# Optimization experiments

Measured on AMD Instinct MI355X. Metric: run time of the kernel, lower is better.

The kernel has to match this reference:

```python
import jax, jax.numpy as jnp
import numpy as np

T, N, D = 64, 40, 4
H, R, K = 256, 64, 2
E = N * (N - 1)


def _xavier(key, shape):
    std = (2.0 / (shape[0] + shape[1])) ** 0.5
    return (std * jax.random.normal(key, shape)).astype(jnp.float32)


def setup_inputs() -> dict:
    ks = iter(jax.random.split(jax.random.key(0), 40))
    send, recv = np.where(np.ones((N, N)) - np.eye(N))  # fully-connected directed graph, E = N*(N-1)
    p = {}
    p['inputs'] = jax.random.normal(next(ks), (1, T, N, D), dtype=jnp.float32)
    p['node_masks'] = jnp.ones((1, T, N), dtype=jnp.float32)
    p['send_edges'] = jnp.asarray(send, dtype=jnp.int32)
    p['recv_edges'] = jnp.asarray(recv, dtype=jnp.int32)
    for name, nin in (('mlp1', D), ('mlp2', 2 * H), ('mlp3', H), ('mlp4', 3 * H)):
        p[name + '_W1'] = _xavier(next(ks), (H, nin))
        p[name + '_b1'] = jnp.full((H,), 0.1, jnp.float32)
        p[name + '_W2'] = _xavier(next(ks), (H, H))
        p[name + '_b2'] = jnp.full((H,), 0.1, jnp.float32)
    s = float(1.0 / np.sqrt(R))
    for nm in ('fwd', 'rev'):
        p[nm + '_Wih'] = jax.random.uniform(next(ks), (4 * R, H), jnp.float32, -s, s)
        p[nm + '_Whh'] = jax.random.uniform(next(ks), (4 * R, R), jnp.float32, -s, s)
        p[nm + '_bih'] = jnp.zeros((4 * R,), jnp.float32)
        p[nm + '_bhh'] = jnp.zeros((4 * R,), jnp.float32)
    p['enc_W'] = _xavier(next(ks), (K, 2 * R))
    p['enc_b'] = jnp.full((K,), 0.1, jnp.float32)
    p['prior_W'] = _xavier(next(ks), (K, R))
    p['prior_b'] = jnp.full((K,), 0.1, jnp.float32)
    return p


def _mlp(x, W1, b1, W2, b2):
    # RefNRIMLP in eval mode with no_bn=True: elu(fc2(elu(fc1(x))))
    return jax.nn.elu(jax.nn.elu(x @ W1.T + b1) @ W2.T + b2)


def _lstm(xs, Wih, Whh, bih, bhh):
    # xs: [T, E, H] -> hidden states [T, E, R]; PyTorch LSTM gate order i, f, g, o
    def step(carry, xt):
        h, c = carry
        g = xt @ Wih.T + bih + h @ Whh.T + bhh
        i, f, gg, o = jnp.split(g, 4, axis=-1)
        c = jax.nn.sigmoid(f) * c + jax.nn.sigmoid(i) * jnp.tanh(gg)
        h = jax.nn.sigmoid(o) * jnp.tanh(c)
        return (h, c), h
    Rh = Whh.shape[1]
    init = (jnp.zeros((xs.shape[1], Rh), xs.dtype), jnp.zeros((xs.shape[1], Rh), xs.dtype))
    _, hs = jax.lax.scan(step, init, xs)
    return hs


def _encode(inputs, send, recv,
            m1W1, m1b1, m1W2, m1b2, m2W1, m2b1, m2W2, m2b2,
            m3W1, m3b1, m3W2, m3b2, m4W1, m4b1, m4W2, m4b2,
            fWih, fWhh, fbih, fbhh, rWih, rWhh, rbih, rbhh,
            encW, encb, priW, prib):
    x = inputs[0]                                                  # [T, N, D]
    h = _mlp(x, m1W1, m1b1, m1W2, m1b2)                            # [T, N, H]
    e = jnp.concatenate([h[:, send], h[:, recv]], axis=-1)         # node2edge gather [T, E, 2H]
    e = _mlp(e, m2W1, m2b1, m2W2, m2b2)                            # [T, E, H]
    skip = e
    n = jnp.zeros((x.shape[0], x.shape[1], e.shape[-1]), e.dtype)
    n = n.at[:, recv].add(e)                                       # edge2node scatter-add (index_add_)
    n = _mlp(n, m3W1, m3b1, m3W2, m3b2)                            # [T, N, H]
    e = jnp.concatenate([n[:, send], n[:, recv], skip], axis=-1)   # [T, E, 3H]
    e = _mlp(e, m4W1, m4b1, m4W2, m4b2)                            # per-edge features over time [T, E, H]
    fwd_h = _lstm(e, fWih, fWhh, fbih, fbhh)                       # [T, E, R]
    rev_h = _lstm(e[::-1], rWih, rWhh, rbih, rbhh)[::-1]           # [T, E, R]
    prior = fwd_h @ priW.T + prib                                  # [T, E, K]
    enc = jnp.concatenate([fwd_h, rev_h], axis=-1) @ encW.T + encb # [T, E, K]
    return jnp.concatenate([prior, enc], axis=-1)                  # [T, E, 2K]


def reference(inputs, node_masks, send_edges, recv_edges,
              mlp1_W1, mlp1_b1, mlp1_W2, mlp1_b2,
              mlp2_W1, mlp2_b1, mlp2_W2, mlp2_b2,
              mlp3_W1, mlp3_b1, mlp3_W2, mlp3_b2,
              mlp4_W1, mlp4_b1, mlp4_W2, mlp4_b2,
              fwd_Wih, fwd_Whh, fwd_bih, fwd_bhh,
              rev_Wih, rev_Whh, rev_bih, rev_bhh,
              enc_W, enc_b, prior_W, prior_b):
    del node_masks  # all nodes present -> static fully-connected graph each step
    return _encode(inputs, send_edges, recv_edges,
                   mlp1_W1, mlp1_b1, mlp1_W2, mlp1_b2,
                   mlp2_W1, mlp2_b1, mlp2_W2, mlp2_b2,
                   mlp3_W1, mlp3_b1, mlp3_W2, mlp3_b2,
                   mlp4_W1, mlp4_b1, mlp4_W2, mlp4_b2,
                   fwd_Wih, fwd_Whh, fwd_bih, fwd_bhh,
                   rev_Wih, rev_Whh, rev_bih, rev_bhh,
                   enc_W, enc_b, prior_W, prior_b)
```

## Files before the change

kernel.cpp:

```cpp
#include <hip/hip_runtime.h>
#include <math.h>

#define T_ 64
#define N_ 40
#define D_ 4
#define H_ 256
#define R_ 64
#define E_ 1560
#define TE_ (T_*E_)
#define TN_ (T_*N_)

typedef unsigned short us;
typedef short short8 __attribute__((ext_vector_type(8)));
typedef float f32x4 __attribute__((ext_vector_type(4)));

__device__ __forceinline__ float elu_f(float x){ return x > 0.f ? x : (__expf(x) - 1.f); }
__device__ __forceinline__ float sig_f(float x){ return 1.f/(1.f+__expf(-x)); }
__device__ __forceinline__ float tanh_f(float x){ return 2.f/(1.f+__expf(-2.f*x)) - 1.f; }
__device__ __forceinline__ float dot4(float4 a, float4 b){ return a.x*b.x + a.y*b.y + a.z*b.z + a.w*b.w; }

__device__ __forceinline__ float bf2f(us u){ return __uint_as_float(((unsigned int)u) << 16); }
__device__ __forceinline__ us f2bf(float f){
    unsigned int u = __float_as_uint(f);
    u += 0x7FFFu + ((u >> 16) & 1u);
    return (us)(u >> 16);
}
__device__ __forceinline__ float4 ld4f(const float* p){ return *(const float4*)p; }
__device__ __forceinline__ float4 ld4f(const us* p){
    ushort4 v = *(const ushort4*)p;
    return make_float4(bf2f(v.x), bf2f(v.y), bf2f(v.z), bf2f(v.w));
}
__device__ __forceinline__ void st4f(float* p, float4 v){ *(float4*)p = v; }
__device__ __forceinline__ void st4f(us* p, float4 v){
    ushort4 o; o.x = f2bf(v.x); o.y = f2bf(v.y); o.z = f2bf(v.z); o.w = f2bf(v.w);
    *(ushort4*)p = o;
}

__device__ __forceinline__ void gld16(void* lds, const void* g){
    __builtin_amdgcn_global_load_lds((const __attribute__((address_space(1))) unsigned int*)g,
                                     (__attribute__((address_space(3))) unsigned int*)lds,
                                     16, 0, 0);
}

__device__ __forceinline__ void wsplit1(const float* W, us* hi, us* lo, int i){
    const float w = W[i];
    const us h = f2bf(w);
    hi[i] = h;
    lo[i] = f2bf(w - bf2f(h));
}

__global__ __launch_bounds__(256)
void wsplit_all(const float* __restrict__ s0, us* h0, us* l0,
                const float* __restrict__ s1, us* h1, us* l1,
                const float* __restrict__ s2, us* h2, us* l2,
                const float* __restrict__ s3, us* h3, us* l3,
                const float* __restrict__ s4, us* h4, us* l4,
                const float* __restrict__ s5, us* h5, us* l5,
                const float* __restrict__ s6, us* h6, us* l6)
{
    int i = blockIdx.x * 256 + threadIdx.x;
    if (i < 65536) { wsplit1(s0, h0, l0, i); return; } i -= 65536;
    if (i < 65536) {
        const float w = s1[(i >> 8) * 768 + 512 + (i & 255)];
        const us h = f2bf(w);
        h1[i] = h;
        l1[i] = f2bf(w - bf2f(h));
        return;
    } i -= 65536;
    if (i < 65536) { wsplit1(s2, h2, l2, i); return; } i -= 65536;
    if (i < 65536) { wsplit1(s3, h3, l3, i); return; } i -= 65536;
    if (i < 65536) { wsplit1(s4, h4, l4, i); return; } i -= 65536;
    if (i < 16384) { wsplit1(s5, h5, l5, i); return; } i -= 16384;
    wsplit1(s6, h6, l6, i);
}

__global__ __launch_bounds__(256)
void mlp1_kernel(const float* __restrict__ x,
                 const float* __restrict__ W1, const float* __restrict__ b1,
                 const float* __restrict__ W2, const float* __restrict__ b2,
                 us* __restrict__ hout)
{
    __shared__ float xs[8][4];
    __shared__ float h1[8][256];
    const int tid = threadIdx.x;
    const int r0  = blockIdx.x * 8;

    if (tid < 32) xs[tid >> 2][tid & 3] = x[r0 * 4 + tid];
    __syncthreads();

    const float4 w1 = *(const float4*)&W1[tid * 4];
    const float bb1 = b1[tid];
    #pragma unroll
    for (int row = 0; row < 8; ++row) {
        float v = bb1 + xs[row][0]*w1.x + xs[row][1]*w1.y + xs[row][2]*w1.z + xs[row][3]*w1.w;
        h1[row][tid] = elu_f(v);
    }
    __syncthreads();

    float acc[8];
    const float bb2 = b2[tid];
    #pragma unroll
    for (int row = 0; row < 8; ++row) acc[row] = bb2;
    const float* w2row = W2 + (size_t)tid * 256;
    for (int k4 = 0; k4 < 64; ++k4) {
        const float4 w = *(const float4*)&w2row[k4 * 4];
        #pragma unroll
        for (int row = 0; row < 8; ++row) {
            const float4 hh = *(const float4*)&h1[row][k4 * 4];
            acc[row] += dot4(hh, w);
        }
    }
    #pragma unroll
    for (int row = 0; row < 8; ++row)
        hout[(size_t)(r0 + row) * 256 + tid] = f2bf(elu_f(acc[row]));
}

__global__ __launch_bounds__(256)
void node_proj(const us* __restrict__ A, const float* __restrict__ W,
               int wstride, float* __restrict__ P)
{
    __shared__ float As[16][64];
    __shared__ float Ws[16][64];

    const int tid  = threadIdx.x;
    const int am   = tid >> 2;
    const int gm   = blockIdx.x * 64 + am;
    const int part = blockIdx.y >> 2;
    const int wq   = blockIdx.y & 3;

    const us* aptr = A + (size_t)gm * 256;
    const float* wptr = W + (size_t)(wq * 64 + am) * wstride + part * 256;

    const int tx = tid & 15, ty = tid >> 4;
    float acc[4][4] = {};

    for (int k0 = 0; k0 < 256; k0 += 16) {
        const float4 a4 = ld4f(aptr + k0 + (tid & 3) * 4);
        const float4 w4 = *(const float4*)(wptr + k0 + (tid & 3) * 4);

        __syncthreads();
        const int ak = (tid & 3) * 4;
        As[ak+0][am] = a4.x; As[ak+1][am] = a4.y; As[ak+2][am] = a4.z; As[ak+3][am] = a4.w;
        Ws[ak+0][am] = w4.x; Ws[ak+1][am] = w4.y; Ws[ak+2][am] = w4.z; Ws[ak+3][am] = w4.w;
        __syncthreads();

        #pragma unroll
        for (int kq = 0; kq < 16; ++kq) {
            const float4 av = *(const float4*)&As[kq][ty * 4];
            const float4 wv = *(const float4*)&Ws[kq][tx * 4];
            const float a_[4] = {av.x, av.y, av.z, av.w};
            const float w_[4] = {wv.x, wv.y, wv.z, wv.w};
            #pragma unroll
            for (int i = 0; i < 4; ++i)
                #pragma unroll
                for (int j = 0; j < 4; ++j)
                    acc[i][j] += a_[i] * w_[j];
        }
    }

    const int gn = part * 256 + wq * 64 + tx * 4;
    #pragma unroll
    for (int i = 0; i < 4; ++i) {
        const int row = blockIdx.x * 64 + ty * 4 + i;
        float4 o;
        o.x = acc[i][0]; o.y = acc[i][1]; o.z = acc[i][2]; o.w = acc[i][3];
        *(float4*)(P + (size_t)row * 512 + gn) = o;
    }
}

__global__ __launch_bounds__(256)
void edge_gather_elu(const float* __restrict__ P, const float* __restrict__ b1,
                     const int* __restrict__ send, const int* __restrict__ recv,
                     us* __restrict__ out)
{
    const int tid = threadIdx.x;
    const int r   = blockIdx.x * 4 + (tid >> 6);
    const int c4  = (tid & 63) * 4;
    const int t = r / E_;
    const int e = r - t * E_;
    const float4 a  = *(const float4*)(P + ((size_t)(t * N_ + send[e])) * 512 + c4);
    const float4 b  = *(const float4*)(P + ((size_t)(t * N_ + recv[e])) * 512 + 256 + c4);
    const float4 bb = *(const float4*)(b1 + c4);
    float4 v;
    v.x = elu_f(a.x + b.x + bb.x);
    v.y = elu_f(a.y + b.y + bb.y);
    v.z = elu_f(a.z + b.z + bb.z);
    v.w = elu_f(a.w + b.w + bb.w);
    ushort4 o; o.x = f2bf(v.x); o.y = f2bf(v.y); o.z = f2bf(v.z); o.w = f2bf(v.w);
    *(ushort4*)(out + (size_t)r * 256 + c4) = o;
}

#define LGKM0 0xC07F
#define VM0   0x3F70
#define VM4   0x3F74

__global__ __launch_bounds__(512, 1)
void gemm_bf(const us* __restrict__ A, const us* __restrict__ WH, const us* __restrict__ WL,
             const float* __restrict__ bias, us* __restrict__ C)
{
    __shared__ char smem[131072];
    char* AG = smem;
    char* WS = smem + 65536;

    const int tid = threadIdx.x, lane = tid & 63, w = tid >> 6;
    const int ml = lane & 15, q = lane >> 4;
    const int lr = lane >> 2;
    const int cofs = (((lane & 3) ^ ((lane >> 3) & 3)) * 8);
    const int qs16 = (q ^ ((ml >> 1) & 3)) * 16;
    const int bx = blockIdx.x;

    char* myWS = WS + w * 8192;
    const size_t wrow0 = (size_t)((w * 2 + 0) * 16 + lr) * 256 + cofs;
    const size_t wrow1 = (size_t)((w * 2 + 1) * 16 + lr) * 256 + cofs;

    #pragma unroll
    for (int g = 0; g < 8; ++g)
        gld16(AG + w * 8192 + g * 1024,
              A + (size_t)(bx * 128 + g * 16 + lr) * 256 + w * 32 + cofs);
    __builtin_amdgcn_s_waitcnt(VM0);
    __syncthreads();

    f32x4 acc[2][8];
    #pragma unroll
    for (int mt = 0; mt < 2; ++mt)
        #pragma unroll
        for (int nt = 0; nt < 8; ++nt) acc[mt][nt] = (f32x4){0.f,0.f,0.f,0.f};

    gld16(myWS +    0, WH + wrow0);
    gld16(myWS + 1024, WH + wrow1);
    gld16(myWS + 2048, WL + wrow0);
    gld16(myWS + 3072, WL + wrow1);

    for (int k = 0; k < 8; ++k) {
        char* cur = myWS + (k & 1) * 4096;
        char* nxt = myWS + ((k + 1) & 1) * 4096;
        if (k < 7) {
            const int k0 = (k + 1) * 32;
            gld16(nxt,        WH + wrow0 + k0);
            gld16(nxt + 1024, WH + wrow1 + k0);
            gld16(nxt + 2048, WL + wrow0 + k0);
            gld16(nxt + 3072, WL + wrow1 + k0);
            __builtin_amdgcn_s_waitcnt(VM4);
        } else {
            __builtin_amdgcn_s_waitcnt(VM0);
        }
        __builtin_amdgcn_sched_barrier(0);
        short8 wh[2], wl[2], ef[8];
        wh[0] = *(const short8*)(cur +        ml*64 + qs16);
        wh[1] = *(const short8*)(cur + 1024 + ml*64 + qs16);
        wl[0] = *(const short8*)(cur + 2048 + ml*64 + qs16);
        wl[1] = *(const short8*)(cur + 3072 + ml*64 + qs16);
        #pragma unroll
        for (int nt = 0; nt < 8; ++nt)
            ef[nt] = *(const short8*)(AG + k*8192 + nt*1024 + ml*64 + qs16);
        __builtin_amdgcn_s_setprio(1);
        #pragma unroll
        for (int nt = 0; nt < 8; ++nt)
            #pragma unroll
            for (int mt = 0; mt < 2; ++mt) {
                acc[mt][nt] = __builtin_amdgcn_mfma_f32_16x16x32_bf16(wh[mt], ef[nt], acc[mt][nt], 0,0,0);
                acc[mt][nt] = __builtin_amdgcn_mfma_f32_16x16x32_bf16(wl[mt], ef[nt], acc[mt][nt], 0,0,0);
            }
        __builtin_amdgcn_s_setprio(0);
        __builtin_amdgcn_s_waitcnt(LGKM0);
        __builtin_amdgcn_sched_barrier(0);
    }

    #pragma unroll
    for (int mt = 0; mt < 2; ++mt) {
        const int col = w * 32 + mt * 16 + q * 4;
        const float4 bb = *(const float4*)(bias + col);
        #pragma unroll
        for (int nt = 0; nt < 8; ++nt) {
            const int row = bx * 128 + nt * 16 + ml;
            float4 v;
            v.x = elu_f(acc[mt][nt][0] + bb.x); v.y = elu_f(acc[mt][nt][1] + bb.y);
            v.z = elu_f(acc[mt][nt][2] + bb.z); v.w = elu_f(acc[mt][nt][3] + bb.w);
            ushort4 o; o.x = f2bf(v.x); o.y = f2bf(v.y); o.z = f2bf(v.z); o.w = f2bf(v.w);
            *(ushort4*)(C + (size_t)row * 256 + col) = o;
        }
    }
}

__global__ __launch_bounds__(512, 1)
void fused_m4(const us* __restrict__ Askip,
              const us* __restrict__ w4aH, const us* __restrict__ w4aL, const float* __restrict__ m4b1,
              const us* __restrict__ w4bH, const us* __restrict__ w4bL, const float* __restrict__ m4b2,
              const us* __restrict__ wfiH, const us* __restrict__ wfiL,
              const float* __restrict__ fbih, const float* __restrict__ fbhh,
              const us* __restrict__ wriH, const us* __restrict__ wriL,
              const float* __restrict__ rbih, const float* __restrict__ rbhh,
              const float* __restrict__ Ptab, const int* __restrict__ send, const int* __restrict__ recv,
              us* __restrict__ Gf, us* __restrict__ Gr)
{
    __shared__ char smem[131072];
    char* AG = smem;
    char* WS = smem + 65536;

    const int tid = threadIdx.x, lane = tid & 63, w = tid >> 6;
    const int ml = lane & 15, q = lane >> 4;
    const int lr = lane >> 2;
    const int cofs = (((lane & 3) ^ ((lane >> 3) & 3)) * 8);
    const int qs16 = (q ^ ((ml >> 1) & 3)) * 16;
    const int bx = blockIdx.x;

    char* myWS = WS + w * 8192;
    const size_t wrow0 = (size_t)((w * 2 + 0) * 16 + lr) * 256 + cofs;
    const size_t wrow1 = (size_t)((w * 2 + 1) * 16 + lr) * 256 + cofs;

    int gtOf[2];
    #pragma unroll
    for (int mt = 0; mt < 2; ++mt)
        gtOf[mt] = w * 8192 + ml * 64 + (((mt * 2 + (q >> 1)) ^ ((ml >> 1) & 3)) * 16) + (q & 1) * 8;

    f32x4 acc[2][8];

    auto runUnit = [&](const us* WH, const us* WL) {
        #pragma unroll
        for (int mt = 0; mt < 2; ++mt)
            #pragma unroll
            for (int nt = 0; nt < 8; ++nt) acc[mt][nt] = (f32x4){0.f,0.f,0.f,0.f};
        gld16(myWS +    0, WH + wrow0);
        gld16(myWS + 1024, WH + wrow1);
        gld16(myWS + 2048, WL + wrow0);
        gld16(myWS + 3072, WL + wrow1);
        for (int k = 0; k < 8; ++k) {
            char* cur = myWS + (k & 1) * 4096;
            char* nxt = myWS + ((k + 1) & 1) * 4096;
            if (k < 7) {
                const int k0 = (k + 1) * 32;
                gld16(nxt,        WH + wrow0 + k0);
                gld16(nxt + 1024, WH + wrow1 + k0);
                gld16(nxt + 2048, WL + wrow0 + k0);
                gld16(nxt + 3072, WL + wrow1 + k0);
                __builtin_amdgcn_s_waitcnt(VM4);
            } else {
                __builtin_amdgcn_s_waitcnt(VM0);
            }
            __builtin_amdgcn_sched_barrier(0);
            short8 wh[2], wl[2], ef[8];
            wh[0] = *(const short8*)(cur +        ml*64 + qs16);
            wh[1] = *(const short8*)(cur + 1024 + ml*64 + qs16);
            wl[0] = *(const short8*)(cur + 2048 + ml*64 + qs16);
            wl[1] = *(const short8*)(cur + 3072 + ml*64 + qs16);
            #pragma unroll
            for (int nt = 0; nt < 8; ++nt)
                ef[nt] = *(const short8*)(AG + k*8192 + nt*1024 + ml*64 + qs16);
            __builtin_amdgcn_s_setprio(1);
            #pragma unroll
            for (int nt = 0; nt < 8; ++nt)
                #pragma unroll
                for (int mt = 0; mt < 2; ++mt) {
                    acc[mt][nt] = __builtin_amdgcn_mfma_f32_16x16x32_bf16(wh[mt], ef[nt], acc[mt][nt], 0,0,0);
                    acc[mt][nt] = __builtin_amdgcn_mfma_f32_16x16x32_bf16(wl[mt], ef[nt], acc[mt][nt], 0,0,0);
                }
            __builtin_amdgcn_s_setprio(0);
            __builtin_amdgcn_s_waitcnt(LGKM0);
            __builtin_amdgcn_sched_barrier(0);
        }
    };

    #pragma unroll
    for (int g = 0; g < 8; ++g)
        gld16(AG + w * 8192 + g * 1024,
              Askip + (size_t)(bx * 128 + g * 16 + lr) * 256 + w * 32 + cofs);
    __builtin_amdgcn_s_waitcnt(VM0);
    __syncthreads();

    ushort4 r16[2][8];

    runUnit(w4aH, w4aL);
    {
        int srw[8], rrw[8];
        #pragma unroll
        for (int nt = 0; nt < 8; ++nt) {
            const int row = bx * 128 + nt * 16 + ml;
            const int t = row / E_;
            const int e = row - t * E_;
            srw[nt] = t * N_ + send[e];
            rrw[nt] = t * N_ + recv[e];
        }
        #pragma unroll
        for (int mt = 0; mt < 2; ++mt) {
            const int col = w * 32 + mt * 16 + q * 4;
            const float4 bb = *(const float4*)(m4b1 + col);
            #pragma unroll
            for (int nt = 0; nt < 8; ++nt) {
                float4 v;
                v.x = acc[mt][nt][0] + bb.x; v.y = acc[mt][nt][1] + bb.y;
                v.z = acc[mt][nt][2] + bb.z; v.w = acc[mt][nt][3] + bb.w;
                const float4 pS = *(const float4*)(Ptab + (size_t)srw[nt] * 512 + col);
                const float4 pR = *(const float4*)(Ptab + (size_t)rrw[nt] * 512 + 256 + col);
                v.x += pS.x + pR.x; v.y += pS.y + pR.y;
                v.z += pS.z + pR.z; v.w += pS.w + pR.w;
                v.x = elu_f(v.x); v.y = elu_f(v.y); v.z = elu_f(v.z); v.w = elu_f(v.w);
                ushort4 o; o.x = f2bf(v.x); o.y = f2bf(v.y); o.z = f2bf(v.z); o.w = f2bf(v.w);
                r16[mt][nt] = o;
            }
        }
    }
    __syncthreads();
    #pragma unroll
    for (int mt = 0; mt < 2; ++mt)
        #pragma unroll
        for (int nt = 0; nt < 8; ++nt)
            *(ushort4*)(AG + gtOf[mt] + nt * 1024) = r16[mt][nt];
    __syncthreads();

    runUnit(w4bH, w4bL);
    #pragma unroll
    for (int mt = 0; mt < 2; ++mt) {
        const int col = w * 32 + mt * 16 + q * 4;
        const float4 bb = *(const float4*)(m4b2 + col);
        #pragma unroll
        for (int nt = 0; nt < 8; ++nt) {
            float4 v;
            v.x = elu_f(acc[mt][nt][0] + bb.x); v.y = elu_f(acc[mt][nt][1] + bb.y);
            v.z = elu_f(acc[mt][nt][2] + bb.z); v.w = elu_f(acc[mt][nt][3] + bb.w);
            ushort4 o; o.x = f2bf(v.x); o.y = f2bf(v.y); o.z = f2bf(v.z); o.w = f2bf(v.w);
            r16[mt][nt] = o;
        }
    }
    __syncthreads();
    #pragma unroll
    for (int mt = 0; mt < 2; ++mt)
        #pragma unroll
        for (int nt = 0; nt < 8; ++nt)
            *(ushort4*)(AG + gtOf[mt] + nt * 1024) = r16[mt][nt];
    __syncthreads();

    runUnit(wfiH, wfiL);
    #pragma unroll
    for (int mt = 0; mt < 2; ++mt) {
        const int col = w * 32 + mt * 16 + q * 4;
        float4 bb = *(const float4*)(fbih + col);
        const float4 b2 = *(const float4*)(fbhh + col);
        bb.x += b2.x; bb.y += b2.y; bb.z += b2.z; bb.w += b2.w;
        #pragma unroll
        for (int nt = 0; nt < 8; ++nt) {
            const int row = bx * 128 + nt * 16 + ml;
            float4 v;
            v.x = acc[mt][nt][0] + bb.x; v.y = acc[mt][nt][1] + bb.y;
            v.z = acc[mt][nt][2] + bb.z; v.w = acc[mt][nt][3] + bb.w;
            ushort4 o; o.x = f2bf(v.x); o.y = f2bf(v.y); o.z = f2bf(v.z); o.w = f2bf(v.w);
            *(ushort4*)(Gf + (size_t)row * 256 + col) = o;
        }
    }

    runUnit(wriH, wriL);
    #pragma unroll
    for (int mt = 0; mt < 2; ++mt) {
        const int col = w * 32 + mt * 16 + q * 4;
        float4 bb = *(const float4*)(rbih + col);
        const float4 b2 = *(const float4*)(rbhh + col);
        bb.x += b2.x; bb.y += b2.y; bb.z += b2.z; bb.w += b2.w;
        #pragma unroll
        for (int nt = 0; nt < 8; ++nt) {
            const int row = bx * 128 + nt * 16 + ml;
            float4 v;
            v.x = acc[mt][nt][0] + bb.x; v.y = acc[mt][nt][1] + bb.y;
            v.z = acc[mt][nt][2] + bb.z; v.w = acc[mt][nt][3] + bb.w;
            ushort4 o; o.x = f2bf(v.x); o.y = f2bf(v.y); o.z = f2bf(v.z); o.w = f2bf(v.w);
            *(ushort4*)(Gr + (size_t)row * 256 + col) = o;
        }
    }
}

template<bool DOELU, typename TA, typename TC>
__global__ __launch_bounds__(256)
void gemm_nt(const TA* __restrict__ A, const float* __restrict__ W,
             const float* __restrict__ bias1,
             TC* __restrict__ C, int M, int Kdim)
{
    __shared__ float As[16][64];
    __shared__ float Ws[16][64];

    const int tid = threadIdx.x;
    const int am  = tid >> 2;
    const int ak  = (tid & 3) * 4;
    const int gm  = blockIdx.x * 64 + am;

    const TA* aptr0 = A + (size_t)gm * Kdim;
    const float* wptr = W + (size_t)(blockIdx.y * 64 + am) * Kdim;

    const int tx = tid & 15, ty = tid >> 4;
    float acc[4][4] = {};

    for (int k0 = 0; k0 < Kdim; k0 += 16) {
        const float4 a4 = ld4f(aptr0 + k0 + ak);
        const float4 w4 = *(const float4*)(wptr + k0 + (tid & 3) * 4);

        __syncthreads();
        As[ak+0][am] = a4.x; As[ak+1][am] = a4.y; As[ak+2][am] = a4.z; As[ak+3][am] = a4.w;
        const int wk = (tid & 3) * 4;
        Ws[wk+0][am] = w4.x; Ws[wk+1][am] = w4.y; Ws[wk+2][am] = w4.z; Ws[wk+3][am] = w4.w;
        __syncthreads();

        #pragma unroll
        for (int kq = 0; kq < 16; ++kq) {
            const float4 av = *(const float4*)&As[kq][ty * 4];
            const float4 wv = *(const float4*)&Ws[kq][tx * 4];
            const float a_[4] = {av.x, av.y, av.z, av.w};
            const float w_[4] = {wv.x, wv.y, wv.z, wv.w};
            #pragma unroll
            for (int i = 0; i < 4; ++i)
                #pragma unroll
                for (int j = 0; j < 4; ++j)
                    acc[i][j] += a_[i] * w_[j];
        }
    }

    const int gn = blockIdx.y * 64 + tx * 4;
    const float4 bb = *(const float4*)&bias1[gn];
    #pragma unroll
    for (int i = 0; i < 4; ++i) {
        const int row = blockIdx.x * 64 + ty * 4 + i;
        float4 o;
        o.x = acc[i][0] + bb.x; o.y = acc[i][1] + bb.y;
        o.z = acc[i][2] + bb.z; o.w = acc[i][3] + bb.w;
        if (DOELU) { o.x = elu_f(o.x); o.y = elu_f(o.y); o.z = elu_f(o.z); o.w = elu_f(o.w); }
        st4f(C + (size_t)row * 256 + gn, o);
    }
}

__global__ __launch_bounds__(256)
void aggregate_kernel(const us* __restrict__ eSkip, const int* __restrict__ recv,
                      float* __restrict__ nAgg)
{
    const int t = blockIdx.x / N_;
    const int j = blockIdx.x - t * N_;
    const int c = threadIdx.x;
    const us* basep = eSkip + (size_t)t * E_ * H_ + c;
    float acc = 0.f;
    #pragma unroll
    for (int s = 0; s < N_; ++s) {
        if (s == j) continue;
        const int e = s * (N_ - 1) + (j < s ? j : j - 1);
        acc += bf2f(basep[(size_t)e * H_]);
    }
    nAgg[(size_t)blockIdx.x * H_ + c] = acc;
}

__global__ __launch_bounds__(256)
void lstm_mfma(const us* __restrict__ Gf, const us* __restrict__ Gr,
               const us* __restrict__ fWhhH, const us* __restrict__ fWhhL,
               const us* __restrict__ rWhhH, const us* __restrict__ rWhhL,
               float* __restrict__ hsF, float* __restrict__ hsR)
{
    const int NBD = (E_ + 15) / 16;
    const bool revd = (int)blockIdx.x >= NBD;
    const int blk = revd ? (int)blockIdx.x - NBD : (int)blockIdx.x;
    const int e0 = blk * 16;
    const us* G  = revd ? Gr : Gf;
    const us* WH = revd ? rWhhH : fWhhH;
    const us* WL = revd ? rWhhL : fWhhL;
    float* hs    = revd ? hsR : hsF;

    const int tid  = threadIdx.x;
    const int lane = tid & 63;
    const int w    = tid >> 6;
    const int ml   = lane & 15;
    const int q    = lane >> 4;

    __shared__ us hHi[2][16][72];
    __shared__ us hLo[2][16][72];

    short8 wfh[4][2], wfl[4][2];
    #pragma unroll
    for (int mt = 0; mt < 4; ++mt) {
        const int row = mt * 64 + w * 16 + ml;
        #pragma unroll
        for (int ks = 0; ks < 2; ++ks) {
            wfh[mt][ks] = *(const short8*)(WH + (size_t)row * 64 + ks * 32 + q * 8);
            wfl[mt][ks] = *(const short8*)(WL + (size_t)row * 64 + ks * 32 + q * 8);
        }
    }

    for (int i = tid; i < 16 * 72; i += 256) { (&hHi[0][0][0])[i] = 0; (&hLo[0][0][0])[i] = 0; }

    const int eMF = min(e0 + ml, E_ - 1);
    const bool wr = (e0 + ml) < E_;
    const int gOfs = w * 16 + q * 4;
    float4 cst = make_float4(0.f, 0.f, 0.f, 0.f);

    ushort4 gcur[4], gnxt[4];
    {
        const int tt0 = revd ? (T_ - 1) : 0;
        const us* gp = G + ((size_t)tt0 * E_ + eMF) * 256 + gOfs;
        #pragma unroll
        for (int mt = 0; mt < 4; ++mt) gcur[mt] = *(const ushort4*)(gp + mt * 64);
    }
    __syncthreads();

    for (int s = 0; s < T_; ++s) {
        const int tt = revd ? (T_ - 1 - s) : s;
        {
            const int sn = (s + 1 < T_) ? s + 1 : s;
            const int tn = revd ? (T_ - 1 - sn) : sn;
            const us* gp = G + ((size_t)tn * E_ + eMF) * 256 + gOfs;
            #pragma unroll
            for (int mt = 0; mt < 4; ++mt) gnxt[mt] = *(const ushort4*)(gp + mt * 64);
        }
        const int rb = s & 1, wb = rb ^ 1;
        short8 bh[2], bl[2];
        #pragma unroll
        for (int ks = 0; ks < 2; ++ks) {
            bh[ks] = *(const short8*)(&hHi[rb][ml][ks * 32 + q * 8]);
            bl[ks] = *(const short8*)(&hLo[rb][ml][ks * 32 + q * 8]);
        }
        f32x4 acc[4];
        #pragma unroll
        for (int mt = 0; mt < 4; ++mt) {
            acc[mt][0] = bf2f(gcur[mt].x); acc[mt][1] = bf2f(gcur[mt].y);
            acc[mt][2] = bf2f(gcur[mt].z); acc[mt][3] = bf2f(gcur[mt].w);
            #pragma unroll
            for (int ks = 0; ks < 2; ++ks) {
                acc[mt] = __builtin_amdgcn_mfma_f32_16x16x32_bf16(wfh[mt][ks], bh[ks], acc[mt], 0, 0, 0);
                acc[mt] = __builtin_amdgcn_mfma_f32_16x16x32_bf16(wfh[mt][ks], bl[ks], acc[mt], 0, 0, 0);
                acc[mt] = __builtin_amdgcn_mfma_f32_16x16x32_bf16(wfl[mt][ks], bh[ks], acc[mt], 0, 0, 0);
            }
        }
        float4 hv;
        cst.x = sig_f(acc[1][0])*cst.x + sig_f(acc[0][0])*tanh_f(acc[2][0]); hv.x = sig_f(acc[3][0])*tanh_f(cst.x);
        cst.y = sig_f(acc[1][1])*cst.y + sig_f(acc[0][1])*tanh_f(acc[2][1]); hv.y = sig_f(acc[3][1])*tanh_f(cst.y);
        cst.z = sig_f(acc[1][2])*cst.z + sig_f(acc[0][2])*tanh_f(acc[2][2]); hv.z = sig_f(acc[3][2])*tanh_f(cst.z);
        cst.w = sig_f(acc[1][3])*cst.w + sig_f(acc[0][3])*tanh_f(acc[2][3]); hv.w = sig_f(acc[3][3])*tanh_f(cst.w);
        ushort4 hh4, hl4;
        hh4.x = f2bf(hv.x); hl4.x = f2bf(hv.x - bf2f(hh4.x));
        hh4.y = f2bf(hv.y); hl4.y = f2bf(hv.y - bf2f(hh4.y));
        hh4.z = f2bf(hv.z); hl4.z = f2bf(hv.z - bf2f(hh4.z));
        hh4.w = f2bf(hv.w); hl4.w = f2bf(hv.w - bf2f(hh4.w));
        *(ushort4*)(&hHi[wb][ml][gOfs]) = hh4;
        *(ushort4*)(&hLo[wb][ml][gOfs]) = hl4;
        if (wr)
            *(float4*)(&hs[((size_t)tt * E_ + e0 + ml) * 64 + gOfs]) = hv;
        __syncthreads();
        #pragma unroll
        for (int mt = 0; mt < 4; ++mt) gcur[mt] = gnxt[mt];
    }
}

__global__ __launch_bounds__(256)
void out_kernel(const float* __restrict__ hsF, const float* __restrict__ hsR,
                const float* __restrict__ priW, const float* __restrict__ prib,
                const float* __restrict__ encW, const float* __restrict__ encb,
                float* __restrict__ out)
{
    const int idx = blockIdx.x * 256 + threadIdx.x;
    const float* f = hsF + (size_t)idx * 64;
    const float* r = hsR + (size_t)idx * 64;
    float p0 = prib[0], p1 = prib[1], q0 = encb[0], q1 = encb[1];
    #pragma unroll
    for (int k4 = 0; k4 < 16; ++k4) {
        const float4 fv = *(const float4*)(f + k4 * 4);
        const float4 rv = *(const float4*)(r + k4 * 4);
        p0 += dot4(fv, *(const float4*)(priW + k4 * 4));
        p1 += dot4(fv, *(const float4*)(priW + 64 + k4 * 4));
        q0 += dot4(fv, *(const float4*)(encW + k4 * 4))
            + dot4(rv, *(const float4*)(encW + 64 + k4 * 4));
        q1 += dot4(fv, *(const float4*)(encW + 128 + k4 * 4))
            + dot4(rv, *(const float4*)(encW + 192 + k4 * 4));
    }
    float4 o; o.x = p0; o.y = p1; o.z = q0; o.w = q1;
    *(float4*)(out + (size_t)idx * 4) = o;
}

extern "C" void kernel_launch(void* const* d_in, const int* in_sizes, int n_in,
                              void* d_out, int out_size, void* d_ws, size_t ws_size,
                              hipStream_t stream)
{
    const float* x    = (const float*)d_in[0];
    const int*   send = (const int*)d_in[2];
    const int*   recv = (const int*)d_in[3];
    const float* m1W1 = (const float*)d_in[4];  const float* m1b1 = (const float*)d_in[5];
    const float* m1W2 = (const float*)d_in[6];  const float* m1b2 = (const float*)d_in[7];
    const float* m2W1 = (const float*)d_in[8];  const float* m2b1 = (const float*)d_in[9];
    const float* m2W2 = (const float*)d_in[10]; const float* m2b2 = (const float*)d_in[11];
    const float* m3W1 = (const float*)d_in[12]; const float* m3b1 = (const float*)d_in[13];
    const float* m3W2 = (const float*)d_in[14]; const float* m3b2 = (const float*)d_in[15];
    const float* m4W1 = (const float*)d_in[16]; const float* m4b1 = (const float*)d_in[17];
    const float* m4W2 = (const float*)d_in[18]; const float* m4b2 = (const float*)d_in[19];
    const float* fWih = (const float*)d_in[20]; const float* fWhh = (const float*)d_in[21];
    const float* fbih = (const float*)d_in[22]; const float* fbhh = (const float*)d_in[23];
    const float* rWih = (const float*)d_in[24]; const float* rWhh = (const float*)d_in[25];
    const float* rbih = (const float*)d_in[26]; const float* rbhh = (const float*)d_in[27];
    const float* encW = (const float*)d_in[28]; const float* encb = (const float*)d_in[29];
    const float* priW = (const float*)d_in[30]; const float* prib = (const float*)d_in[31];

    const size_t SZN  = (size_t)TN_ * H_;
    const size_t SZE  = (size_t)TE_ * H_;
    float* n_agg = (float*)d_ws;
    float* m3t   = n_agg + SZN;
    float* Ptab  = (float*)d_ws;
    us* h16      = (us*)(m3t + SZN);
    us* n3       = h16 + SZN;
    us* w2bH = n3  + SZN;          us* w2bL = w2bH + 65536;
    us* w4aH = w2bL + 65536;       us* w4aL = w4aH + 65536;
    us* w4bH = w4aL + 65536;       us* w4bL = w4bH + 65536;
    us* wfiH = w4bL + 65536;       us* wfiL = wfiH + 65536;
    us* wriH = wfiL + 65536;       us* wriL = wriH + 65536;
    us* whfH = wriL + 65536;       us* whfL = whfH + 16384;
    us* whrH = whfL + 16384;       us* whrL = whrH + 16384;
    us* bufA16 = whrL + 16384;
    us* bufB16 = bufA16 + SZE;
    us* bufC16 = bufB16 + SZE;
    float* hsF = (float*)bufC16;
    float* hsR = hsF + (size_t)TE_ * R_;
    const size_t needed = ((size_t)(bufC16 + SZE) - (size_t)d_ws);
    if (ws_size < needed) return;

    const dim3 gN(TN_ / 64, 4), gNP(TN_ / 64, 8);

    wsplit_all<<<1408, 256, 0, stream>>>(m2W2, w2bH, w2bL,
                                         m4W1, w4aH, w4aL,
                                         m4W2, w4bH, w4bL,
                                         fWih, wfiH, wfiL, rWih, wriH, wriL,
                                         fWhh, whfH, whfL, rWhh, whrH, whrL);

    mlp1_kernel<<<TN_ / 8, 256, 0, stream>>>(x, m1W1, m1b1, m1W2, m1b2, h16);
    node_proj<<<gNP, 256, 0, stream>>>(h16, m2W1, 512, Ptab);
    edge_gather_elu<<<TE_ / 4, 256, 0, stream>>>(Ptab, m2b1, send, recv, bufA16);
    gemm_bf<<<TE_ / 128, 512, 0, stream>>>(bufA16, w2bH, w2bL, m2b2, bufB16);
    aggregate_kernel<<<TN_, 256, 0, stream>>>(bufB16, recv, n_agg);
    gemm_nt<true, float, float><<<gN, 256, 0, stream>>>(n_agg, m3W1, m3b1, m3t, TN_, 256);
    gemm_nt<true, float, us><<<gN, 256, 0, stream>>>(m3t, m3W2, m3b2, n3, TN_, 256);
    node_proj<<<gNP, 256, 0, stream>>>(n3, m4W1, 768, Ptab);
    fused_m4<<<TE_ / 128, 512, 0, stream>>>(bufB16,
                                            w4aH, w4aL, m4b1,
                                            w4bH, w4bL, m4b2,
                                            wfiH, wfiL, fbih, fbhh,
                                            wriH, wriL, rbih, rbhh,
                                            Ptab, send, recv, bufA16, bufB16);
    lstm_mfma<<<2 * ((E_ + 15) / 16), 256, 0, stream>>>(bufA16, bufB16, whfH, whfL, whrH, whrL, hsF, hsR);
    out_kernel<<<TE_ / 256, 256, 0, stream>>>(hsF, hsR, priW, prib, encW, encb, (float*)d_out);
}
```

Baseline: 547.9 us.

## Split edge GEMMs over 16 waves, load weights directly into registers

gemm_bf and fused_m4 now launch 1024 threads per block. Sixteen waves each compute a 64-row by 32-column sub-tile, where before eight waves each computed 128 rows. Weight fragments are read straight from global memory into registers with a two-stage register double buffer, which removes the LDS weight staging, its 64 KB of shared memory and the explicit waitcnt and sched barriers. The aim is more waves in flight to hide latency on the small grid of 780 blocks, at the cost of each wave fetching its own weight fragments from global memory or L2 with no LDS sharing.

```diff
diff --git a/kernel.cpp b/kernel.cpp
--- a/kernel.cpp
+++ b/kernel.cpp
@@ -190,17 +190,13 @@
     *(ushort4*)(out + (size_t)r * 256 + c4) = o;
 }
 
-#define LGKM0 0xC07F
 #define VM0   0x3F70
-#define VM4   0x3F74
-
-__global__ __launch_bounds__(512, 1)
+
+__global__ __launch_bounds__(1024, 4)
 void gemm_bf(const us* __restrict__ A, const us* __restrict__ WH, const us* __restrict__ WL,
              const float* __restrict__ bias, us* __restrict__ C)
 {
-    __shared__ char smem[131072];
-    char* AG = smem;
-    char* WS = smem + 65536;
+    __shared__ char AG[65536];
 
     const int tid = threadIdx.x, lane = tid & 63, w = tid >> 6;
     const int ml = lane & 15, q = lane >> 4;
@@ -208,71 +204,73 @@
     const int cofs = (((lane & 3) ^ ((lane >> 3) & 3)) * 8);
     const int qs16 = (q ^ ((ml >> 1) & 3)) * 16;
     const int bx = blockIdx.x;
-
-    char* myWS = WS + w * 8192;
-    const size_t wrow0 = (size_t)((w * 2 + 0) * 16 + lr) * 256 + cofs;
-    const size_t wrow1 = (size_t)((w * 2 + 1) * 16 + lr) * 256 + cofs;
-
-    #pragma unroll
-    for (int g = 0; g < 8; ++g)
-        gld16(AG + w * 8192 + g * 1024,
-              A + (size_t)(bx * 128 + g * 16 + lr) * 256 + w * 32 + cofs);
+    const int eh = w >> 3;
+    const int fh = w & 7;
+
+    {
+        const int ks = w >> 1;
+        const int gb = (w & 1) * 4;
+        #pragma unroll
+        for (int i = 0; i < 4; ++i)
+            gld16(AG + ks * 8192 + (gb + i) * 1024,
+                  A + (size_t)(bx * 128 + (gb + i) * 16 + lr) * 256 + ks * 32 + cofs);
+    }
     __builtin_amdgcn_s_waitcnt(VM0);
     __syncthreads();
 
-    f32x4 acc[2][8];
+    const us* whp[2]; const us* wlp[2];
+    #pragma unroll
+    for (int mt = 0; mt < 2; ++mt) {
+        const int row = fh * 32 + mt * 16 + ml;
+        whp[mt] = WH + (size_t)row * 256 + q * 8;
+        wlp[mt] = WL + (size_t)row * 256 + q * 8;
+    }
+
+    f32x4 acc[2][4];
     #pragma unroll
     for (int mt = 0; mt < 2; ++mt)
         #pragma unroll
-        for (int nt = 0; nt < 8; ++nt) acc[mt][nt] = (f32x4){0.f,0.f,0.f,0.f};
-
-    gld16(myWS +    0, WH + wrow0);
-    gld16(myWS + 1024, WH + wrow1);
-    gld16(myWS + 2048, WL + wrow0);
-    gld16(myWS + 3072, WL + wrow1);
-
+        for (int nt = 0; nt < 4; ++nt) acc[mt][nt] = (f32x4){0.f,0.f,0.f,0.f};
+
+    short8 whb[2][2], wlb[2][2];
+    #pragma unroll
+    for (int mt = 0; mt < 2; ++mt) {
+        whb[0][mt] = *(const short8*)whp[mt];
+        wlb[0][mt] = *(const short8*)wlp[mt];
+    }
+
+    #pragma unroll
     for (int k = 0; k < 8; ++k) {
-        char* cur = myWS + (k & 1) * 4096;
-        char* nxt = myWS + ((k + 1) & 1) * 4096;
+        const int cp = k & 1, np = cp ^ 1;
         if (k < 7) {
-            const int k0 = (k + 1) * 32;
-            gld16(nxt,        WH + wrow0 + k0);
-            gld16(nxt + 1024, WH + wrow1 + k0);
-            gld16(nxt + 2048, WL + wrow0 + k0);
-            gld16(nxt + 3072, WL + wrow1 + k0);
-            __builtin_amdgcn_s_waitcnt(VM4);
-        } else {
-            __builtin_amdgcn_s_waitcnt(VM0);
-        }
-        __builtin_amdgcn_sched_barrier(0);
-        short8 wh[2], wl[2], ef[8];
-        wh[0] = *(const short8*)(cur +        ml*64 + qs16);
-        wh[1] = *(const short8*)(cur + 1024 + ml*64 + qs16);
-        wl[0] = *(const short8*)(cur + 2048 + ml*64 + qs16);
-        wl[1] = *(const short8*)(cur + 3072 + ml*64 + qs16);
-        #pragma unroll
-        for (int nt = 0; nt < 8; ++nt)
-            ef[nt] = *(const short8*)(AG + k*8192 + nt*1024 + ml*64 + qs16);
+            #pragma unroll
+            for (int mt = 0; mt < 2; ++mt) {
+                whb[np][mt] = *(const short8*)(whp[mt] + (k + 1) * 32);
+                wlb[np][mt] = *(const short8*)(wlp[mt] + (k + 1) * 32);
+            }
+        }
+        short8 ef[4];
+        #pragma unroll
+        for (int nt = 0; nt < 4; ++nt)
+            ef[nt] = *(const short8*)(AG + k * 8192 + (eh * 4 + nt) * 1024 + ml * 64 + qs16);
         __builtin_amdgcn_s_setprio(1);
         #pragma unroll
-        for (int nt = 0; nt < 8; ++nt)
+        for (int nt = 0; nt < 4; ++nt)
             #pragma unroll
             for (int mt = 0; mt < 2; ++mt) {
-                acc[mt][nt] = __builtin_amdgcn_mfma_f32_16x16x32_bf16(wh[mt], ef[nt], acc[mt][nt], 0,0,0);
-                acc[mt][nt] = __builtin_amdgcn_mfma_f32_16x16x32_bf16(wl[mt], ef[nt], acc[mt][nt], 0,0,0);
+                acc[mt][nt] = __builtin_amdgcn_mfma_f32_16x16x32_bf16(whb[cp][mt], ef[nt], acc[mt][nt], 0,0,0);
+                acc[mt][nt] = __builtin_amdgcn_mfma_f32_16x16x32_bf16(wlb[cp][mt], ef[nt], acc[mt][nt], 0,0,0);
             }
         __builtin_amdgcn_s_setprio(0);
-        __builtin_amdgcn_s_waitcnt(LGKM0);
-        __builtin_amdgcn_sched_barrier(0);
     }
 
     #pragma unroll
     for (int mt = 0; mt < 2; ++mt) {
-        const int col = w * 32 + mt * 16 + q * 4;
+        const int col = fh * 32 + mt * 16 + q * 4;
         const float4 bb = *(const float4*)(bias + col);
         #pragma unroll
-        for (int nt = 0; nt < 8; ++nt) {
-            const int row = bx * 128 + nt * 16 + ml;
+        for (int nt = 0; nt < 4; ++nt) {
+            const int row = bx * 128 + eh * 64 + nt * 16 + ml;
             float4 v;
             v.x = elu_f(acc[mt][nt][0] + bb.x); v.y = elu_f(acc[mt][nt][1] + bb.y);
             v.z = elu_f(acc[mt][nt][2] + bb.z); v.w = elu_f(acc[mt][nt][3] + bb.w);
@@ -282,7 +280,7 @@
     }
 }
 
-__global__ __launch_bounds__(512, 1)
+__global__ __launch_bounds__(1024, 4)
 void fused_m4(const us* __restrict__ Askip,
               const us* __restrict__ w4aH, const us* __restrict__ w4aL, const float* __restrict__ m4b1,
               const us* __restrict__ w4bH, const us* __restrict__ w4bL, const float* __restrict__ m4b2,
@@ -293,9 +291,7 @@
               const float* __restrict__ Ptab, const int* __restrict__ send, const int* __restrict__ recv,
               us* __restrict__ Gf, us* __restrict__ Gr)
 {
-    __shared__ char smem[131072];
-    char* AG = smem;
-    char* WS = smem + 65536;
+    __shared__ char AG[65536];
 
     const int tid = threadIdx.x, lane = tid & 63, w = tid >> 6;
     const int ml = lane & 15, q = lane >> 4;
@@ -303,78 +299,79 @@
     const int cofs = (((lane & 3) ^ ((lane >> 3) & 3)) * 8);
     const int qs16 = (q ^ ((ml >> 1) & 3)) * 16;
     const int bx = blockIdx.x;
-
-    char* myWS = WS + w * 8192;
-    const size_t wrow0 = (size_t)((w * 2 + 0) * 16 + lr) * 256 + cofs;
-    const size_t wrow1 = (size_t)((w * 2 + 1) * 16 + lr) * 256 + cofs;
+    const int eh = w >> 3;
+    const int fh = w & 7;
 
     int gtOf[2];
     #pragma unroll
     for (int mt = 0; mt < 2; ++mt)
-        gtOf[mt] = w * 8192 + ml * 64 + (((mt * 2 + (q >> 1)) ^ ((ml >> 1) & 3)) * 16) + (q & 1) * 8;
-
-    f32x4 acc[2][8];
-
-    auto runUnit = [&](const us* WH, const us* WL) {
+        gtOf[mt] = fh * 8192 + ml * 64 + (((mt * 2 + (q >> 1)) ^ ((ml >> 1) & 3)) * 16) + (q & 1) * 8;
+
+    f32x4 acc[2][4];
+
+    auto runUnit = [&](const us* __restrict__ WHm, const us* __restrict__ WLm) {
         #pragma unroll
         for (int mt = 0; mt < 2; ++mt)
             #pragma unroll
-            for (int nt = 0; nt < 8; ++nt) acc[mt][nt] = (f32x4){0.f,0.f,0.f,0.f};
-        gld16(myWS +    0, WH + wrow0);
-        gld16(myWS + 1024, WH + wrow1);
-        gld16(myWS + 2048, WL + wrow0);
-        gld16(myWS + 3072, WL + wrow1);
+            for (int nt = 0; nt < 4; ++nt) acc[mt][nt] = (f32x4){0.f,0.f,0.f,0.f};
+        const us* whp[2]; const us* wlp[2];
+        #pragma unroll
+        for (int mt = 0; mt < 2; ++mt) {
+            const int row = fh * 32 + mt * 16 + ml;
+            whp[mt] = WHm + (size_t)row * 256 + q * 8;
+            wlp[mt] = WLm + (size_t)row * 256 + q * 8;
+        }
+        short8 whb[2][2], wlb[2][2];
+        #pragma unroll
+        for (int mt = 0; mt < 2; ++mt) {
+            whb[0][mt] = *(const short8*)whp[mt];
+            wlb[0][mt] = *(const short8*)wlp[mt];
+        }
+        #pragma unroll
         for (int k = 0; k < 8; ++k) {
-            char* cur = myWS + (k & 1) * 4096;
-            char* nxt = myWS + ((k + 1) & 1) * 4096;
+            const int cp = k & 1, np = cp ^ 1;
             if (k < 7) {
-                const int k0 = (k + 1) * 32;
-                gld16(nxt,        WH + wrow0 + k0);
-                gld16(nxt + 1024, WH + wrow1 + k0);
-                gld16(nxt + 2048, WL + wrow0 + k0);
-                gld16(nxt + 3072, WL + wrow1 + k0);
-                __builtin_amdgcn_s_waitcnt(VM4);
-            } else {
-                __builtin_amdgcn_s_waitcnt(VM0);
-            }
-            __builtin_amdgcn_sched_barrier(0);
-            short8 wh[2], wl[2], ef[8];
-            wh[0] = *(const short8*)(cur +        ml*64 + qs16);
-            wh[1] = *(const short8*)(cur + 1024 + ml*64 + qs16);
-            wl[0] = *(const short8*)(cur + 2048 + ml*64 + qs16);
-            wl[1] = *(const short8*)(cur + 3072 + ml*64 + qs16);
-            #pragma unroll
-            for (int nt = 0; nt < 8; ++nt)
-                ef[nt] = *(const short8*)(AG + k*8192 + nt*1024 + ml*64 + qs16);
-            __builtin_amdgcn_s_setprio(1);
-            #pragma unroll
-            for (int nt = 0; nt < 8; ++nt)
                 #pragma unroll
                 for (int mt = 0; mt < 2; ++mt) {
-                    acc[mt][nt] = __builtin_amdgcn_mfma_f32_16x16x32_bf16(wh[mt], ef[nt], acc[mt][nt], 0,0,0);
-                    acc[mt][nt] = __builtin_amdgcn_mfma_f32_16x16x32_bf16(wl[mt], ef[nt], acc[mt][nt], 0,0,0);
+                    whb[np][mt] = *(const short8*)(whp[mt] + (k + 1) * 32);
+                    wlb[np][mt] = *(const short8*)(wlp[mt] + (k + 1) * 32);
+                }
+            }
+            short8 ef[4];
+            #pragma unroll
+            for (int nt = 0; nt < 4; ++nt)
+                ef[nt] = *(const short8*)(AG + k * 8192 + (eh * 4 + nt) * 1024 + ml * 64 + qs16);
+            __builtin_amdgcn_s_setprio(1);
+            #pragma unroll
+            for (int nt = 0; nt < 4; ++nt)
+                #pragma unroll
+                for (int mt = 0; mt < 2; ++mt) {
+                    acc[mt][nt] = __builtin_amdgcn_mfma_f32_16x16x32_bf16(whb[cp][mt], ef[nt], acc[mt][nt], 0,0,0);
+                    acc[mt][nt] = __builtin_amdgcn_mfma_f32_16x16x32_bf16(wlb[cp][mt], ef[nt], acc[mt][nt], 0,0,0);
                 }
             __builtin_amdgcn_s_setprio(0);
-            __builtin_amdgcn_s_waitcnt(LGKM0);
-            __builtin_amdgcn_sched_barrier(0);
         }
     };
 
-    #pragma unroll
-    for (int g = 0; g < 8; ++g)
-        gld16(AG + w * 8192 + g * 1024,
-              Askip + (size_t)(bx * 128 + g * 16 + lr) * 256 + w * 32 + cofs);
+    {
+        const int ks = w >> 1;
+        const int gb = (w & 1) * 4;
+        #pragma unroll
+        for (int i = 0; i < 4; ++i)
+            gld16(AG + ks * 8192 + (gb + i) * 1024,
+                  Askip + (size_t)(bx * 128 + (gb + i) * 16 + lr) * 256 + ks * 32 + cofs);
+    }
     __builtin_amdgcn_s_waitcnt(VM0);
     __syncthreads();
 
-    ushort4 r16[2][8];
+    ushort4 r16[2][4];
 
     runUnit(w4aH, w4aL);
     {
-        int srw[8], rrw[8];
-        #pragma unroll
-        for (int nt = 0; nt < 8; ++nt) {
-            const int row = bx * 128 + nt * 16 + ml;
+        int srw[4], rrw[4];
+        #pragma unroll
+        for (int nt = 0; nt < 4; ++nt) {
+            const int row = bx * 128 + eh * 64 + nt * 16 + ml;
             const int t = row / E_;
             const int e = row - t * E_;
             srw[nt] = t * N_ + send[e];
@@ -382,10 +379,10 @@
         }
         #pragma unroll
         for (int mt = 0; mt < 2; ++mt) {
-            const int col = w * 32 + mt * 16 + q * 4;
+            const int col = fh * 32 + mt * 16 + q * 4;
             const float4 bb = *(const float4*)(m4b1 + col);
             #pragma unroll
-            for (int nt = 0; nt < 8; ++nt) {
+            for (int nt = 0; nt < 4; ++nt) {
                 float4 v;
                 v.x = acc[mt][nt][0] + bb.x; v.y = acc[mt][nt][1] + bb.y;
                 v.z = acc[mt][nt][2] + bb.z; v.w = acc[mt][nt][3] + bb.w;
@@ -403,17 +400,17 @@
     #pragma unroll
     for (int mt = 0; mt < 2; ++mt)
         #pragma unroll
-        for (int nt = 0; nt < 8; ++nt)
-            *(ushort4*)(AG + gtOf[mt] + nt * 1024) = r16[mt][nt];
+        for (int nt = 0; nt < 4; ++nt)
+            *(ushort4*)(AG + gtOf[mt] + (eh * 4 + nt) * 1024) = r16[mt][nt];
     __syncthreads();
 
     runUnit(w4bH, w4bL);
     #pragma unroll
     for (int mt = 0; mt < 2; ++mt) {
-        const int col = w * 32 + mt * 16 + q * 4;
+        const int col = fh * 32 + mt * 16 + q * 4;
         const float4 bb = *(const float4*)(m4b2 + col);
         #pragma unroll
-        for (int nt = 0; nt < 8; ++nt) {
+        for (int nt = 0; nt < 4; ++nt) {
             float4 v;
             v.x = elu_f(acc[mt][nt][0] + bb.x); v.y = elu_f(acc[mt][nt][1] + bb.y);
             v.z = elu_f(acc[mt][nt][2] + bb.z); v.w = elu_f(acc[mt][nt][3] + bb.w);
@@ -425,20 +422,20 @@
     #pragma unroll
     for (int mt = 0; mt < 2; ++mt)
         #pragma unroll
-        for (int nt = 0; nt < 8; ++nt)
-            *(ushort4*)(AG + gtOf[mt] + nt * 1024) = r16[mt][nt];
+        for (int nt = 0; nt < 4; ++nt)
+            *(ushort4*)(AG + gtOf[mt] + (eh * 4 + nt) * 1024) = r16[mt][nt];
     __syncthreads();
 
     runUnit(wfiH, wfiL);
     #pragma unroll
     for (int mt = 0; mt < 2; ++mt) {
-        const int col = w * 32 + mt * 16 + q * 4;
+        const int col = fh * 32 + mt * 16 + q * 4;
         float4 bb = *(const float4*)(fbih + col);
         const float4 b2 = *(const float4*)(fbhh + col);
         bb.x += b2.x; bb.y += b2.y; bb.z += b2.z; bb.w += b2.w;
         #pragma unroll
-        for (int nt = 0; nt < 8; ++nt) {
-            const int row = bx * 128 + nt * 16 + ml;
+        for (int nt = 0; nt < 4; ++nt) {
+            const int row = bx * 128 + eh * 64 + nt * 16 + ml;
             float4 v;
             v.x = acc[mt][nt][0] + bb.x; v.y = acc[mt][nt][1] + bb.y;
             v.z = acc[mt][nt][2] + bb.z; v.w = acc[mt][nt][3] + bb.w;
@@ -450,13 +447,13 @@
     runUnit(wriH, wriL);
     #pragma unroll
     for (int mt = 0; mt < 2; ++mt) {
-        const int col = w * 32 + mt * 16 + q * 4;
+        const int col = fh * 32 + mt * 16 + q * 4;
         float4 bb = *(const float4*)(rbih + col);
         const float4 b2 = *(const float4*)(rbhh + col);
         bb.x += b2.x; bb.y += b2.y; bb.z += b2.z; bb.w += b2.w;
         #pragma unroll
-        for (int nt = 0; nt < 8; ++nt) {
-            const int row = bx * 128 + nt * 16 + ml;
+        for (int nt = 0; nt < 4; ++nt) {
+            const int row = bx * 128 + eh * 64 + nt * 16 + ml;
             float4 v;
             v.x = acc[mt][nt][0] + bb.x; v.y = acc[mt][nt][1] + bb.y;
             v.z = acc[mt][nt][2] + bb.z; v.w = acc[mt][nt][3] + bb.w;
@@ -720,17 +717,17 @@
     mlp1_kernel<<<TN_ / 8, 256, 0, stream>>>(x, m1W1, m1b1, m1W2, m1b2, h16);
     node_proj<<<gNP, 256, 0, stream>>>(h16, m2W1, 512, Ptab);
     edge_gather_elu<<<TE_ / 4, 256, 0, stream>>>(Ptab, m2b1, send, recv, bufA16);
-    gemm_bf<<<TE_ / 128, 512, 0, stream>>>(bufA16, w2bH, w2bL, m2b2, bufB16);
+    gemm_bf<<<TE_ / 128, 1024, 0, stream>>>(bufA16, w2bH, w2bL, m2b2, bufB16);
     aggregate_kernel<<<TN_, 256, 0, stream>>>(bufB16, recv, n_agg);
     gemm_nt<true, float, float><<<gN, 256, 0, stream>>>(n_agg, m3W1, m3b1, m3t, TN_, 256);
     gemm_nt<true, float, us><<<gN, 256, 0, stream>>>(m3t, m3W2, m3b2, n3, TN_, 256);
     node_proj<<<gNP, 256, 0, stream>>>(n3, m4W1, 768, Ptab);
-    fused_m4<<<TE_ / 128, 512, 0, stream>>>(bufB16,
-                                            w4aH, w4aL, m4b1,
-                                            w4bH, w4bL, m4b2,
-                                            wfiH, wfiL, fbih, fbhh,
-                                            wriH, wriL, rbih, rbhh,
-                                            Ptab, send, recv, bufA16, bufB16);
+    fused_m4<<<TE_ / 128, 1024, 0, stream>>>(bufB16,
+                                             w4aH, w4aL, m4b1,
+                                             w4bH, w4bL, m4b2,
+                                             wfiH, wfiL, fbih, fbhh,
+                                             wriH, wriL, rbih, rbhh,
+                                             Ptab, send, recv, bufA16, bufB16);
     lstm_mfma<<<2 * ((E_ + 15) / 16), 256, 0, stream>>>(bufA16, bufB16, whfH, whfL, whrH, whrL, hsF, hsR);
     out_kernel<<<TE_ / 256, 256, 0, stream>>>(hsF, hsR, priW, prib, encW, encb, (float*)d_out);
 }
```

Measured after the change: 711.8 us. 1.3x slower.
